# Performance work log

Measured on AMD Instinct MI355X. Metric: run time of the kernel, lower is better.

The kernel has to match this reference:

```python
import jax, jax.numpy as jnp
import numpy as np

H = 16  # num_heads
EPS = 1e-12  # F.normalize eps


def setup_inputs() -> dict:
    key = jax.random.key(0)
    ks = jax.random.split(key, 7)
    B, L, D = 2, 2048, 1024
    s = 0.02  # small init scale for numerical sanity
    return {
        "x": jax.random.normal(ks[0], (B, L, D), dtype=jnp.float32),
        "Wq": jax.random.normal(ks[1], (D, D), dtype=jnp.float32) * s,
        "Wk": jax.random.normal(ks[2], (D, D), dtype=jnp.float32) * s,
        "Wv": jax.random.normal(ks[3], (D, D), dtype=jnp.float32) * s,
        "Wo": jax.random.normal(ks[4], (D, D), dtype=jnp.float32) * s,
        "Wb": jax.random.normal(ks[5], (D, H), dtype=jnp.float32) * s,
        "bb": jnp.zeros((H,), dtype=jnp.float32),
    }


def _l2norm(t):
    # matches torch F.normalize(p=2, dim=-1): x / max(||x||, eps)
    n = jnp.sqrt(jnp.sum(t * t, axis=-1, keepdims=True))
    return t / jnp.maximum(n, EPS)


def reference(x, Wq, Wk, Wv, Wo, Wb, bb):
    B, L, Dm = x.shape
    Dh = Dm // H
    q = (x @ Wq).reshape(B, L, H, Dh)
    k = (x @ Wk).reshape(B, L, H, Dh)
    v = (x @ Wv).reshape(B, L, H, Dh)
    beta = jax.nn.sigmoid(x @ Wb + bb)  # [B, L, H]
    q = _l2norm(q)
    k = _l2norm(k)
    # out[b,l,h,e] = sum_{t<=l} beta[b,t,h] * <q[b,l,h], k[b,t,h]> * v[b,t,h,e]
    # Exact reformulation of the cumsum-of-outer-products in the source,
    # avoiding the B*L*H*Dh*Dh state blow-up.
    scores = jnp.einsum('blhd,bthd->bhlt', q, k)
    scores = scores * beta.transpose(0, 2, 1)[:, :, None, :]  # scale by beta_t
    mask = jnp.tril(jnp.ones((L, L), dtype=scores.dtype))  # causal incl. diagonal
    scores = scores * mask
    out = jnp.einsum('bhlt,bthe->blhe', scores, v).reshape(B, L, Dm)
    return out @ Wo
```

## Files before the change

kernel.cpp:

```cpp
#include <hip/hip_runtime.h>
#include <stdint.h>

#define DEV static __device__ __forceinline__

typedef __bf16 bf16x8 __attribute__((ext_vector_type(8)));
typedef unsigned short u16x8 __attribute__((ext_vector_type(8)));
typedef float f32x4 __attribute__((ext_vector_type(4)));

DEV unsigned short f2bf(float f) {
    unsigned int u = __builtin_bit_cast(unsigned int, f);
    u = (u + 0x7FFFu + ((u >> 16) & 1u)) >> 16;
    return (unsigned short)u;
}
DEV float bf2f(unsigned short h) {
    unsigned int u = ((unsigned int)h) << 16;
    return __builtin_bit_cast(float, u);
}

DEV void gload_lds16(const unsigned short* g, unsigned short* l) {
    __builtin_amdgcn_global_load_lds(
        (const __attribute__((address_space(1))) unsigned int*)g,
        (__attribute__((address_space(3))) unsigned int*)l, 16, 0, 0);
}

__global__ __launch_bounds__(256) void k_prep(
    const float* __restrict__ x, const float* __restrict__ Wq,
    const float* __restrict__ Wk, const float* __restrict__ Wv,
    const float* __restrict__ Wo, const float* __restrict__ Wb,
    const float* __restrict__ bb, unsigned short* __restrict__ xb,
    unsigned short* __restrict__ Wqkvt, unsigned short* __restrict__ Wot,
    float* __restrict__ beta) {
    __shared__ __align__(16) char smem[65536];
    int bid = blockIdx.x, tid = threadIdx.x;
    if (bid < 4096) {
        int i = bid * 256 + tid;
        float4 v = ((const float4*)x)[i];
        ushort4 o;
        o.x = f2bf(v.x); o.y = f2bf(v.y); o.z = f2bf(v.z); o.w = f2bf(v.w);
        ((ushort4*)xb)[i] = o;
    } else if (bid < 8192) {
        float (*tile)[33] = (float(*)[33])smem;
        int idx = bid - 4096;
        int z = idx >> 10, rem = idx & 1023;
        const float* W = (z == 0) ? Wq : (z == 1) ? Wk : (z == 2) ? Wv : Wo;
        int k0 = (rem & 31) * 32, n0 = (rem >> 5) * 32;
        int tx = tid & 31, ty = tid >> 5;
        #pragma unroll
        for (int r = 0; r < 32; r += 8)
            tile[ty + r][tx] = W[(size_t)(k0 + ty + r) * 1024 + n0 + tx];
        __syncthreads();
        #pragma unroll
        for (int r = 0; r < 32; r += 8) {
            float v = tile[tx][ty + r];
            int n = n0 + ty + r, k = k0 + tx;
            if (z < 3) Wqkvt[(size_t)(z * 1024 + n) * 1024 + k] = f2bf(v);
            else       Wot[(size_t)n * 1024 + k] = f2bf(v);
        }
    } else {
        float* WbT = (float*)smem;
        int bbl = bid - 8192;
        #pragma unroll
        for (int j = 0; j < 16; j++) {
            int idx4 = tid + 256 * j;
            float4 v = ((const float4*)Wb)[idx4];
            int i = idx4 >> 2;
            int h0 = (idx4 & 3) * 4;
            WbT[(h0 + 0) * 1024 + (i ^ ((h0 + 0) << 2))] = v.x;
            WbT[(h0 + 1) * 1024 + (i ^ ((h0 + 1) << 2))] = v.y;
            WbT[(h0 + 2) * 1024 + (i ^ ((h0 + 2) << 2))] = v.z;
            WbT[(h0 + 3) * 1024 + (i ^ ((h0 + 3) << 2))] = v.w;
        }
        __syncthreads();
        int w = tid >> 6, lane = tid & 63;
        #pragma unroll 1
        for (int r = 0; r < 4; r++) {
            int row = bbl * 16 + w * 4 + r;
            const float* xr = x + (size_t)row * 1024;
            float acc[16] = {};
            #pragma unroll
            for (int k = 0; k < 16; k++) {
                int i = lane + 64 * k;
                float xv = xr[i];
                #pragma unroll
                for (int h = 0; h < 16; h++)
                    acc[h] += xv * WbT[h * 1024 + (i ^ (h << 2))];
            }
            #pragma unroll
            for (int h = 0; h < 16; h++) {
                #pragma unroll
                for (int m = 32; m; m >>= 1) acc[h] += __shfl_xor(acc[h], m, 64);
            }
            if (lane == 0) {
                #pragma unroll
                for (int h = 0; h < 16; h++)
                    beta[row * 16 + h] = 1.f / (1.f + __expf(-(acc[h] + bb[h])));
            }
        }
    }
}

__global__ __launch_bounds__(256) void k_gemm_qkv(const unsigned short* __restrict__ A,
                                                  const unsigned short* __restrict__ Bt,
                                                  unsigned short* __restrict__ C) {
    __shared__ unsigned short As[128 * 32];
    __shared__ unsigned short Bs[128 * 32];
    int m0 = blockIdx.x * 128, n0 = blockIdx.y * 128;
    int tid = threadIdx.x;
    int w = tid >> 6, lane = tid & 63, g = lane >> 4, ln = lane & 15;
    int wr = w >> 1, wc = w & 1;
    f32x4 acc[4][4] = {};
    for (int k0 = 0; k0 < 1024; k0 += 32) {
        #pragma unroll
        for (int cc = 0; cc < 2; cc++) {
            int base = (w * 2 + cc) * 64;
            int chunk = base + lane;
            int row = chunk >> 2, ps = chunk & 3;
            int sl = (ps - (row >> 1)) & 3;
            gload_lds16(A + (size_t)(m0 + row) * 1024 + k0 + sl * 8, &As[base * 8]);
            gload_lds16(Bt + (size_t)(n0 + row) * 1024 + k0 + sl * 8, &Bs[base * 8]);
        }
        __syncthreads();
        bf16x8 af[4], bfr[4];
        #pragma unroll
        for (int mi = 0; mi < 4; mi++) {
            int row = wr * 64 + mi * 16 + ln;
            int ps = (g + (row >> 1)) & 3;
            af[mi] = *(const bf16x8*)(&As[row * 32 + ps * 8]);
        }
        #pragma unroll
        for (int ni = 0; ni < 4; ni++) {
            int row = wc * 64 + ni * 16 + ln;
            int ps = (g + (row >> 1)) & 3;
            bfr[ni] = *(const bf16x8*)(&Bs[row * 32 + ps * 8]);
        }
        #pragma unroll
        for (int mi = 0; mi < 4; mi++)
            #pragma unroll
            for (int ni = 0; ni < 4; ni++)
                acc[mi][ni] = __builtin_amdgcn_mfma_f32_16x16x32_bf16(
                    af[mi], bfr[ni], acc[mi][ni], 0, 0, 0);
        __syncthreads();
    }
    #pragma unroll
    for (int mi = 0; mi < 4; mi++)
        #pragma unroll
        for (int ni = 0; ni < 4; ni++)
            #pragma unroll
            for (int r = 0; r < 4; r++) {
                int row = m0 + wr * 64 + mi * 16 + g * 4 + r;
                int col = n0 + wc * 64 + ni * 16 + ln;
                C[(size_t)row * 3072 + col] = f2bf(acc[mi][ni][r]);
            }
}

__global__ __launch_bounds__(256) void k_gemm_out(const unsigned short* __restrict__ A,
                                                  const unsigned short* __restrict__ Bt,
                                                  float* __restrict__ C) {
    __shared__ unsigned short As[128 * 32];
    __shared__ unsigned short Bs[64 * 32];
    int m0 = blockIdx.x * 128, n0 = blockIdx.y * 64;
    int tid = threadIdx.x;
    int w = tid >> 6, lane = tid & 63, g = lane >> 4, ln = lane & 15;
    int wr = w >> 1, wc = w & 1;
    f32x4 acc[4][2] = {};
    for (int k0 = 0; k0 < 1024; k0 += 32) {
        #pragma unroll
        for (int i = 0; i < 3; i++) {
            int base = w * 192 + i * 64;
            int chunk = base + lane;
            if (base < 512) {
                int row = chunk >> 2, ps = chunk & 3;
                int sl = (ps - (row >> 1)) & 3;
                gload_lds16(A + (size_t)(m0 + row) * 1024 + k0 + sl * 8, &As[base * 8]);
            } else {
                int bc = chunk - 512;
                int row = bc >> 2, ps = bc & 3;
                int sl = (ps - (row >> 1)) & 3;
                gload_lds16(Bt + (size_t)(n0 + row) * 1024 + k0 + sl * 8, &Bs[(base - 512) * 8]);
            }
        }
        __syncthreads();
        bf16x8 af[4], bfr[2];
        #pragma unroll
        for (int mi = 0; mi < 4; mi++) {
            int row = wr * 64 + mi * 16 + ln;
            int ps = (g + (row >> 1)) & 3;
            af[mi] = *(const bf16x8*)(&As[row * 32 + ps * 8]);
        }
        #pragma unroll
        for (int ni = 0; ni < 2; ni++) {
            int row = wc * 32 + ni * 16 + ln;
            int ps = (g + (row >> 1)) & 3;
            bfr[ni] = *(const bf16x8*)(&Bs[row * 32 + ps * 8]);
        }
        #pragma unroll
        for (int mi = 0; mi < 4; mi++)
            #pragma unroll
            for (int ni = 0; ni < 2; ni++)
                acc[mi][ni] = __builtin_amdgcn_mfma_f32_16x16x32_bf16(
                    af[mi], bfr[ni], acc[mi][ni], 0, 0, 0);
        __syncthreads();
    }
    #pragma unroll
    for (int mi = 0; mi < 4; mi++)
        #pragma unroll
        for (int ni = 0; ni < 2; ni++)
            #pragma unroll
            for (int r = 0; r < 4; r++) {
                int row = m0 + wr * 64 + mi * 16 + g * 4 + r;
                int col = n0 + wc * 32 + ni * 16 + ln;
                C[(size_t)row * 1024 + col] = acc[mi][ni][r];
            }
}

DEV int vswz(int dh, int ks) { return (ks ^ (dh & 7) ^ ((dh >> 3) & 7)) & 7; }

__global__ __launch_bounds__(256) void k_state(const unsigned short* __restrict__ QKV,
                                               const float* __restrict__ beta,
                                               unsigned short* __restrict__ Mbuf) {
    __shared__ unsigned short Kt[64 * 64];
    __shared__ unsigned short Vt[64 * 64];
    int c = blockIdx.x, bh = blockIdx.y;
    int b = bh >> 4, h = bh & 15;
    int tid = threadIdx.x, w = tid >> 6, lane = tid & 63, g = lane >> 4, ln = lane & 15;
    int row0 = b * 2048 + c * 64;
    const unsigned short* Kg = QKV + 1024;
    const unsigned short* Vg = QKV + 2048;
    #pragma unroll
    for (int cc = 0; cc < 2; cc++) {
        int ci = tid + cc * 256;
        int r = ci >> 3, sl = ci & 7;
        uint4 kd = *(const uint4*)(Kg + (size_t)(row0 + r) * 3072 + h * 64 + sl * 8);
        uint4 vd = *(const uint4*)(Vg + (size_t)(row0 + r) * 3072 + h * 64 + sl * 8);
        union { uint4 q; unsigned short s[8]; } uk, uv;
        uk.q = kd; uv.q = vd;
        float ssk = 0.f;
        #pragma unroll
        for (int i = 0; i < 8; i++) { float v = bf2f(uk.s[i]); ssk += v * v; }
        ssk += __shfl_xor(ssk, 1, 64);
        ssk += __shfl_xor(ssk, 2, 64);
        ssk += __shfl_xor(ssk, 4, 64);
        float ksc = beta[(row0 + r) * 16 + h] / fmaxf(sqrtf(ssk), 1e-12f);
        #pragma unroll
        for (int i = 0; i < 8; i++) {
            int dh = sl * 8 + i;
            int off = dh * 64 + vswz(dh, r >> 3) * 8 + (r & 7);
            Kt[off] = f2bf(bf2f(uk.s[i]) * ksc);
            Vt[off] = uv.s[i];
        }
    }
    __syncthreads();
    f32x4 macc[4] = {};
    #pragma unroll
    for (int st = 0; st < 2; st++) {
        int c0 = st * 32 + g * 4;
        int rk = w * 16 + ln;
        uint2 klo = *(const uint2*)(&Kt[rk * 64 + vswz(rk, c0 >> 3) * 8 + (c0 & 7)]);
        uint2 khi = *(const uint2*)(&Kt[rk * 64 + vswz(rk, (c0 + 16) >> 3) * 8 + (c0 & 7)]);
        uint4 kc = make_uint4(klo.x, klo.y, khi.x, khi.y);
        bf16x8 bfrag = __builtin_bit_cast(bf16x8, kc);
        #pragma unroll
        for (int mt = 0; mt < 4; mt++) {
            int rv = mt * 16 + ln;
            uint2 lo = *(const uint2*)(&Vt[rv * 64 + vswz(rv, c0 >> 3) * 8 + (c0 & 7)]);
            uint2 hi = *(const uint2*)(&Vt[rv * 64 + vswz(rv, (c0 + 16) >> 3) * 8 + (c0 & 7)]);
            uint4 comb = make_uint4(lo.x, lo.y, hi.x, hi.y);
            bf16x8 afrag = __builtin_bit_cast(bf16x8, comb);
            macc[mt] = __builtin_amdgcn_mfma_f32_16x16x32_bf16(afrag, bfrag, macc[mt], 0, 0, 0);
        }
    }
    unsigned short* Mc = Mbuf + ((size_t)bh * 32 + c) * 4096;
    #pragma unroll
    for (int mt = 0; mt < 4; mt++)
        #pragma unroll
        for (int r = 0; r < 4; r++)
            Mc[(mt * 16 + g * 4 + r) * 64 + w * 16 + ln] = f2bf(macc[mt][r]);
}

__global__ __launch_bounds__(256) void k_prefix(unsigned short* __restrict__ Mbuf) {
    int bh = blockIdx.x >> 3, slice = blockIdx.x & 7;
    int base = slice * 512 + threadIdx.x * 2;
    unsigned short* M = Mbuf + (size_t)bh * 32 * 4096 + base;
    unsigned int v[32];
    #pragma unroll
    for (int c = 0; c < 32; c++) v[c] = *(const unsigned int*)(M + (size_t)c * 4096);
    float a0 = 0.f, a1 = 0.f;
    #pragma unroll
    for (int c = 0; c < 32; c++) {
        unsigned int pack = (unsigned int)f2bf(a0) | ((unsigned int)f2bf(a1) << 16);
        *(unsigned int*)(M + (size_t)c * 4096) = pack;
        a0 += bf2f((unsigned short)(v[c] & 0xFFFF));
        a1 += bf2f((unsigned short)(v[c] >> 16));
    }
}

__global__ __launch_bounds__(256) void k_attn2(const unsigned short* __restrict__ QKV,
                                               const unsigned short* __restrict__ Sbuf,
                                               const float* __restrict__ beta,
                                               unsigned short* __restrict__ attn) {
    __shared__ unsigned short Ks[64 * 64];
    __shared__ unsigned short Vt[64 * 64];
    __shared__ unsigned short STs[64 * 64];
    int qt = blockIdx.x, bh = blockIdx.y;
    int b = bh >> 4, h = bh & 15;
    int tid = threadIdx.x, w = tid >> 6, lane = tid & 63, g = lane >> 4, ln = lane & 15;
    int rowbase = b * 2048 + qt * 64;

    const unsigned short* Qrow = QKV + (size_t)(rowbase + w * 16 + ln) * 3072 + h * 64;
    u16x8 qu0 = *(const u16x8*)(Qrow + g * 8);
    u16x8 qu1 = *(const u16x8*)(Qrow + 32 + g * 8);
    bf16x8 qf[2];
    qf[0] = __builtin_bit_cast(bf16x8, qu0);
    qf[1] = __builtin_bit_cast(bf16x8, qu1);
    float ssq = 0.f;
    #pragma unroll
    for (int j = 0; j < 8; j++) {
        float v0 = bf2f(qu0[j]), v1 = bf2f(qu1[j]);
        ssq += v0 * v0 + v1 * v1;
    }
    ssq += __shfl_xor(ssq, 16, 64);
    ssq += __shfl_xor(ssq, 32, 64);
    float qscale = 1.f / fmaxf(sqrtf(ssq), 1e-12f);

    const unsigned short* Kg = QKV + 1024;
    const unsigned short* Vg = QKV + 2048;
    const unsigned short* Sg = Sbuf + ((size_t)bh * 32 + qt) * 4096;

    #pragma unroll
    for (int cc = 0; cc < 2; cc++) {
        int c = tid + cc * 256;
        int r = c >> 3, sl = c & 7;
        uint4 kd = *(const uint4*)(Kg + (size_t)(rowbase + r) * 3072 + h * 64 + sl * 8);
        union { uint4 q; unsigned short s[8]; } uk; uk.q = kd;
        float ssk = 0.f;
        #pragma unroll
        for (int i = 0; i < 8; i++) { float v = bf2f(uk.s[i]); ssk += v * v; }
        ssk += __shfl_xor(ssk, 1, 64);
        ssk += __shfl_xor(ssk, 2, 64);
        ssk += __shfl_xor(ssk, 4, 64);
        float ksc = beta[(rowbase + r) * 16 + h] / fmaxf(sqrtf(ssk), 1e-12f);
        #pragma unroll
        for (int i = 0; i < 8; i++) uk.s[i] = f2bf(bf2f(uk.s[i]) * ksc);
        *(uint4*)(&Ks[r * 64 + ((sl ^ (r & 7)) * 8)]) = uk.q;
        uint4 sd = *(const uint4*)(Sg + r * 64 + sl * 8);
        *(uint4*)(&STs[r * 64 + ((sl ^ (r & 7)) * 8)]) = sd;
        uint4 vd = *(const uint4*)(Vg + (size_t)(rowbase + r) * 3072 + h * 64 + sl * 8);
        union { uint4 q; unsigned short s[8]; } uv; uv.q = vd;
        #pragma unroll
        for (int i = 0; i < 8; i++) {
            int dh = sl * 8 + i;
            Vt[dh * 64 + vswz(dh, r >> 3) * 8 + (r & 7)] = uv.s[i];
        }
    }
    __syncthreads();

    f32x4 oacc[4] = {};

    #pragma unroll
    for (int st = 0; st < 2; st++)
        #pragma unroll
        for (int mt2 = 0; mt2 < 4; mt2++) {
            int r = mt2 * 16 + ln;
            int ps = (st * 4 + g) ^ (r & 7);
            bf16x8 a = *(const bf16x8*)(&STs[r * 64 + ps * 8]);
            oacc[mt2] = __builtin_amdgcn_mfma_f32_16x16x32_bf16(a, qf[st], oacc[mt2], 0, 0, 0);
        }

    f32x4 s[4] = {};
    #pragma unroll
    for (int st = 0; st < 2; st++)
        #pragma unroll
        for (int mt = 0; mt < 4; mt++) {
            int r = mt * 16 + ln;
            int ps = (st * 4 + g) ^ (r & 7);
            bf16x8 a = *(const bf16x8*)(&Ks[r * 64 + ps * 8]);
            s[mt] = __builtin_amdgcn_mfma_f32_16x16x32_bf16(a, qf[st], s[mt], 0, 0, 0);
        }
    {
        int qr = w * 16 + ln;
        #pragma unroll
        for (int mt = 0; mt < 4; mt++)
            #pragma unroll
            for (int r = 0; r < 4; r++)
                if (mt * 16 + g * 4 + r > qr) s[mt][r] = 0.f;
    }
    bf16x8 pf[2];
    #pragma unroll
    for (int st = 0; st < 2; st++) {
        u16x8 t;
        #pragma unroll
        for (int r = 0; r < 4; r++) {
            t[r]     = f2bf(s[2 * st][r]);
            t[4 + r] = f2bf(s[2 * st + 1][r]);
        }
        pf[st] = __builtin_bit_cast(bf16x8, t);
    }
    #pragma unroll
    for (int st = 0; st < 2; st++)
        #pragma unroll
        for (int mt2 = 0; mt2 < 4; mt2++) {
            int rv = mt2 * 16 + ln;
            int c0 = st * 32 + g * 4;
            uint2 lo = *(const uint2*)(&Vt[rv * 64 + vswz(rv, c0 >> 3) * 8 + (c0 & 7)]);
            uint2 hi = *(const uint2*)(&Vt[rv * 64 + vswz(rv, (c0 + 16) >> 3) * 8 + (c0 & 7)]);
            uint4 comb = make_uint4(lo.x, lo.y, hi.x, hi.y);
            bf16x8 a = __builtin_bit_cast(bf16x8, comb);
            oacc[mt2] = __builtin_amdgcn_mfma_f32_16x16x32_bf16(a, pf[st], oacc[mt2], 0, 0, 0);
        }
    __syncthreads();

    {
        int qr = w * 16 + ln;
        #pragma unroll
        for (int mt2 = 0; mt2 < 4; mt2++)
            #pragma unroll
            for (int r = 0; r < 4; r++) {
                int dh = mt2 * 16 + g * 4 + r;
                Ks[qr * 64 + (dh ^ ((qr & 7) << 3))] = f2bf(oacc[mt2][r] * qscale);
            }
    }
    __syncthreads();
    #pragma unroll
    for (int cc = 0; cc < 2; cc++) {
        int c = tid + cc * 256;
        int r = c >> 3, sl = c & 7;
        uint4 d = *(const uint4*)(&Ks[r * 64 + ((sl ^ (r & 7)) * 8)]);
        *(uint4*)(attn + (size_t)(rowbase + r) * 1024 + h * 64 + sl * 8) = d;
    }
}

extern "C" void kernel_launch(void* const* d_in, const int* in_sizes, int n_in,
                              void* d_out, int out_size, void* d_ws, size_t ws_size,
                              hipStream_t stream) {
    const float* x  = (const float*)d_in[0];
    const float* Wq = (const float*)d_in[1];
    const float* Wk = (const float*)d_in[2];
    const float* Wv = (const float*)d_in[3];
    const float* Wo = (const float*)d_in[4];
    const float* Wb = (const float*)d_in[5];
    const float* bb = (const float*)d_in[6];
    float* out = (float*)d_out;

    char* ws = (char*)d_ws;
    unsigned short* xb    = (unsigned short*)(ws);
    unsigned short* Mbuf  = (unsigned short*)(ws);
    unsigned short* Wqkvt = (unsigned short*)(ws + (8ull  << 20));
    unsigned short* Wot   = (unsigned short*)(ws + (14ull << 20));
    unsigned short* QKVb  = (unsigned short*)(ws + (16ull << 20));
    float*          beta  = (float*)         (ws + (40ull << 20));
    unsigned short* attn  = (unsigned short*)(ws + (41ull << 20));

    k_prep<<<8448, 256, 0, stream>>>(x, Wq, Wk, Wv, Wo, Wb, bb, xb, Wqkvt, Wot, beta);
    k_gemm_qkv<<<dim3(32, 24), 256, 0, stream>>>(xb, Wqkvt, QKVb);
    k_state<<<dim3(32, 32), 256, 0, stream>>>(QKVb, beta, Mbuf);
    k_prefix<<<256, 256, 0, stream>>>(Mbuf);
    k_attn2<<<dim3(32, 32), 256, 0, stream>>>(QKVb, Mbuf, beta, attn);
    k_gemm_out<<<dim3(32, 16), 256, 0, stream>>>(attn, Wot, out);
}
```

Baseline: 192.4 us.

## Split prep kernel to shrink LDS, and double GEMM K-tile to 64

Moves the beta projection out of the prep kernel into its own kernel, so the cast/transpose blocks no longer reserve 64KB of LDS and can run at higher occupancy. The beta kernel now uses one row per wave across 1024 blocks. Both GEMMs also stage 64-wide K tiles with an 8-slot swizzle, halving the barrier and loop count per K. The cost is an extra kernel launch and twice the LDS per GEMM block.

```diff
diff --git a/kernel.cpp b/kernel.cpp
--- a/kernel.cpp
+++ b/kernel.cpp
@@ -23,14 +23,12 @@
         (__attribute__((address_space(3))) unsigned int*)l, 16, 0, 0);
 }
 
-__global__ __launch_bounds__(256) void k_prep(
+__global__ __launch_bounds__(256) void k_prep0(
     const float* __restrict__ x, const float* __restrict__ Wq,
     const float* __restrict__ Wk, const float* __restrict__ Wv,
-    const float* __restrict__ Wo, const float* __restrict__ Wb,
-    const float* __restrict__ bb, unsigned short* __restrict__ xb,
-    unsigned short* __restrict__ Wqkvt, unsigned short* __restrict__ Wot,
-    float* __restrict__ beta) {
-    __shared__ __align__(16) char smem[65536];
+    const float* __restrict__ Wo, unsigned short* __restrict__ xb,
+    unsigned short* __restrict__ Wqkvt, unsigned short* __restrict__ Wot) {
+    __shared__ float tile[32][33];
     int bid = blockIdx.x, tid = threadIdx.x;
     if (bid < 4096) {
         int i = bid * 256 + tid;
@@ -38,8 +36,7 @@
         ushort4 o;
         o.x = f2bf(v.x); o.y = f2bf(v.y); o.z = f2bf(v.z); o.w = f2bf(v.w);
         ((ushort4*)xb)[i] = o;
-    } else if (bid < 8192) {
-        float (*tile)[33] = (float(*)[33])smem;
+    } else {
         int idx = bid - 4096;
         int z = idx >> 10, rem = idx & 1023;
         const float* W = (z == 0) ? Wq : (z == 1) ? Wk : (z == 2) ? Wv : Wo;
@@ -56,89 +53,94 @@
             if (z < 3) Wqkvt[(size_t)(z * 1024 + n) * 1024 + k] = f2bf(v);
             else       Wot[(size_t)n * 1024 + k] = f2bf(v);
         }
-    } else {
-        float* WbT = (float*)smem;
-        int bbl = bid - 8192;
-        #pragma unroll
-        for (int j = 0; j < 16; j++) {
-            int idx4 = tid + 256 * j;
-            float4 v = ((const float4*)Wb)[idx4];
-            int i = idx4 >> 2;
-            int h0 = (idx4 & 3) * 4;
-            WbT[(h0 + 0) * 1024 + (i ^ ((h0 + 0) << 2))] = v.x;
-            WbT[(h0 + 1) * 1024 + (i ^ ((h0 + 1) << 2))] = v.y;
-            WbT[(h0 + 2) * 1024 + (i ^ ((h0 + 2) << 2))] = v.z;
-            WbT[(h0 + 3) * 1024 + (i ^ ((h0 + 3) << 2))] = v.w;
-        }
-        __syncthreads();
-        int w = tid >> 6, lane = tid & 63;
-        #pragma unroll 1
-        for (int r = 0; r < 4; r++) {
-            int row = bbl * 16 + w * 4 + r;
-            const float* xr = x + (size_t)row * 1024;
-            float acc[16] = {};
-            #pragma unroll
-            for (int k = 0; k < 16; k++) {
-                int i = lane + 64 * k;
-                float xv = xr[i];
-                #pragma unroll
-                for (int h = 0; h < 16; h++)
-                    acc[h] += xv * WbT[h * 1024 + (i ^ (h << 2))];
-            }
-            #pragma unroll
-            for (int h = 0; h < 16; h++) {
-                #pragma unroll
-                for (int m = 32; m; m >>= 1) acc[h] += __shfl_xor(acc[h], m, 64);
-            }
-            if (lane == 0) {
-                #pragma unroll
-                for (int h = 0; h < 16; h++)
-                    beta[row * 16 + h] = 1.f / (1.f + __expf(-(acc[h] + bb[h])));
-            }
-        }
+    }
+}
+
+__global__ __launch_bounds__(256) void k_beta(const float* __restrict__ x,
+                                              const float* __restrict__ Wb,
+                                              const float* __restrict__ bb,
+                                              float* __restrict__ beta) {
+    __shared__ float WbT[16 * 1024];
+    int tid = threadIdx.x;
+    #pragma unroll
+    for (int j = 0; j < 16; j++) {
+        int idx4 = tid + 256 * j;
+        float4 v = ((const float4*)Wb)[idx4];
+        int i = idx4 >> 2;
+        int h0 = (idx4 & 3) * 4;
+        WbT[(h0 + 0) * 1024 + (i ^ ((h0 + 0) << 2))] = v.x;
+        WbT[(h0 + 1) * 1024 + (i ^ ((h0 + 1) << 2))] = v.y;
+        WbT[(h0 + 2) * 1024 + (i ^ ((h0 + 2) << 2))] = v.z;
+        WbT[(h0 + 3) * 1024 + (i ^ ((h0 + 3) << 2))] = v.w;
+    }
+    __syncthreads();
+    int w = tid >> 6, lane = tid & 63;
+    int row = blockIdx.x * 4 + w;
+    const float* xr = x + (size_t)row * 1024;
+    float acc[16] = {};
+    #pragma unroll
+    for (int k = 0; k < 16; k++) {
+        int i = lane + 64 * k;
+        float xv = xr[i];
+        #pragma unroll
+        for (int h = 0; h < 16; h++)
+            acc[h] += xv * WbT[h * 1024 + (i ^ (h << 2))];
+    }
+    #pragma unroll
+    for (int h = 0; h < 16; h++) {
+        #pragma unroll
+        for (int m = 32; m; m >>= 1) acc[h] += __shfl_xor(acc[h], m, 64);
+    }
+    if (lane == 0) {
+        #pragma unroll
+        for (int h = 0; h < 16; h++)
+            beta[row * 16 + h] = 1.f / (1.f + __expf(-(acc[h] + bb[h])));
     }
 }
 
 __global__ __launch_bounds__(256) void k_gemm_qkv(const unsigned short* __restrict__ A,
                                                   const unsigned short* __restrict__ Bt,
                                                   unsigned short* __restrict__ C) {
-    __shared__ unsigned short As[128 * 32];
-    __shared__ unsigned short Bs[128 * 32];
+    __shared__ unsigned short As[128 * 64];
+    __shared__ unsigned short Bs[128 * 64];
     int m0 = blockIdx.x * 128, n0 = blockIdx.y * 128;
     int tid = threadIdx.x;
     int w = tid >> 6, lane = tid & 63, g = lane >> 4, ln = lane & 15;
     int wr = w >> 1, wc = w & 1;
     f32x4 acc[4][4] = {};
-    for (int k0 = 0; k0 < 1024; k0 += 32) {
-        #pragma unroll
-        for (int cc = 0; cc < 2; cc++) {
-            int base = (w * 2 + cc) * 64;
+    for (int k0 = 0; k0 < 1024; k0 += 64) {
+        #pragma unroll
+        for (int cc = 0; cc < 4; cc++) {
+            int base = (w * 4 + cc) * 64;
             int chunk = base + lane;
-            int row = chunk >> 2, ps = chunk & 3;
-            int sl = (ps - (row >> 1)) & 3;
+            int row = chunk >> 3, ps = chunk & 7;
+            int sl = (ps - (row >> 1)) & 7;
             gload_lds16(A + (size_t)(m0 + row) * 1024 + k0 + sl * 8, &As[base * 8]);
             gload_lds16(Bt + (size_t)(n0 + row) * 1024 + k0 + sl * 8, &Bs[base * 8]);
         }
         __syncthreads();
-        bf16x8 af[4], bfr[4];
-        #pragma unroll
-        for (int mi = 0; mi < 4; mi++) {
-            int row = wr * 64 + mi * 16 + ln;
-            int ps = (g + (row >> 1)) & 3;
-            af[mi] = *(const bf16x8*)(&As[row * 32 + ps * 8]);
-        }
-        #pragma unroll
-        for (int ni = 0; ni < 4; ni++) {
-            int row = wc * 64 + ni * 16 + ln;
-            int ps = (g + (row >> 1)) & 3;
-            bfr[ni] = *(const bf16x8*)(&Bs[row * 32 + ps * 8]);
-        }
-        #pragma unroll
-        for (int mi = 0; mi < 4; mi++)
-            #pragma unroll
-            for (int ni = 0; ni < 4; ni++)
-                acc[mi][ni] = __builtin_amdgcn_mfma_f32_16x16x32_bf16(
-                    af[mi], bfr[ni], acc[mi][ni], 0, 0, 0);
+        #pragma unroll
+        for (int s = 0; s < 2; s++) {
+            bf16x8 af[4], bfr[4];
+            #pragma unroll
+            for (int mi = 0; mi < 4; mi++) {
+                int row = wr * 64 + mi * 16 + ln;
+                int ps = (s * 4 + g + (row >> 1)) & 7;
+                af[mi] = *(const bf16x8*)(&As[row * 64 + ps * 8]);
+            }
+            #pragma unroll
+            for (int ni = 0; ni < 4; ni++) {
+                int row = wc * 64 + ni * 16 + ln;
+                int ps = (s * 4 + g + (row >> 1)) & 7;
+                bfr[ni] = *(const bf16x8*)(&Bs[row * 64 + ps * 8]);
+            }
+            #pragma unroll
+            for (int mi = 0; mi < 4; mi++)
+                #pragma unroll
+                for (int ni = 0; ni < 4; ni++)
+                    acc[mi][ni] = __builtin_amdgcn_mfma_f32_16x16x32_bf16(
+                        af[mi], bfr[ni], acc[mi][ni], 0, 0, 0);
+        }
         __syncthreads();
     }
     #pragma unroll
@@ -156,49 +158,52 @@
 __global__ __launch_bounds__(256) void k_gemm_out(const unsigned short* __restrict__ A,
                                                   const unsigned short* __restrict__ Bt,
                                                   float* __restrict__ C) {
-    __shared__ unsigned short As[128 * 32];
-    __shared__ unsigned short Bs[64 * 32];
+    __shared__ unsigned short As[128 * 64];
+    __shared__ unsigned short Bs[64 * 64];
     int m0 = blockIdx.x * 128, n0 = blockIdx.y * 64;
     int tid = threadIdx.x;
     int w = tid >> 6, lane = tid & 63, g = lane >> 4, ln = lane & 15;
     int wr = w >> 1, wc = w & 1;
     f32x4 acc[4][2] = {};
-    for (int k0 = 0; k0 < 1024; k0 += 32) {
-        #pragma unroll
-        for (int i = 0; i < 3; i++) {
-            int base = w * 192 + i * 64;
+    for (int k0 = 0; k0 < 1024; k0 += 64) {
+        #pragma unroll
+        for (int i = 0; i < 6; i++) {
+            int base = w * 384 + i * 64;
             int chunk = base + lane;
-            if (base < 512) {
-                int row = chunk >> 2, ps = chunk & 3;
-                int sl = (ps - (row >> 1)) & 3;
+            if (base < 1024) {
+                int row = chunk >> 3, ps = chunk & 7;
+                int sl = (ps - (row >> 1)) & 7;
                 gload_lds16(A + (size_t)(m0 + row) * 1024 + k0 + sl * 8, &As[base * 8]);
             } else {
-                int bc = chunk - 512;
-                int row = bc >> 2, ps = bc & 3;
-                int sl = (ps - (row >> 1)) & 3;
-                gload_lds16(Bt + (size_t)(n0 + row) * 1024 + k0 + sl * 8, &Bs[(base - 512) * 8]);
+                int bc = chunk - 1024;
+                int row = bc >> 3, ps = bc & 7;
+                int sl = (ps - (row >> 1)) & 7;
+                gload_lds16(Bt + (size_t)(n0 + row) * 1024 + k0 + sl * 8, &Bs[(base - 1024) * 8]);
             }
         }
         __syncthreads();
-        bf16x8 af[4], bfr[2];
-        #pragma unroll
-        for (int mi = 0; mi < 4; mi++) {
-            int row = wr * 64 + mi * 16 + ln;
-            int ps = (g + (row >> 1)) & 3;
-            af[mi] = *(const bf16x8*)(&As[row * 32 + ps * 8]);
-        }
-        #pragma unroll
-        for (int ni = 0; ni < 2; ni++) {
-            int row = wc * 32 + ni * 16 + ln;
-            int ps = (g + (row >> 1)) & 3;
-            bfr[ni] = *(const bf16x8*)(&Bs[row * 32 + ps * 8]);
-        }
-        #pragma unroll
-        for (int mi = 0; mi < 4; mi++)
-            #pragma unroll
-            for (int ni = 0; ni < 2; ni++)
-                acc[mi][ni] = __builtin_amdgcn_mfma_f32_16x16x32_bf16(
-                    af[mi], bfr[ni], acc[mi][ni], 0, 0, 0);
+        #pragma unroll
+        for (int s = 0; s < 2; s++) {
+            bf16x8 af[4], bfr[2];
+            #pragma unroll
+            for (int mi = 0; mi < 4; mi++) {
+                int row = wr * 64 + mi * 16 + ln;
+                int ps = (s * 4 + g + (row >> 1)) & 7;
+                af[mi] = *(const bf16x8*)(&As[row * 64 + ps * 8]);
+            }
+            #pragma unroll
+            for (int ni = 0; ni < 2; ni++) {
+                int row = wc * 32 + ni * 16 + ln;
+                int ps = (s * 4 + g + (row >> 1)) & 7;
+                bfr[ni] = *(const bf16x8*)(&Bs[row * 64 + ps * 8]);
+            }
+            #pragma unroll
+            for (int mi = 0; mi < 4; mi++)
+                #pragma unroll
+                for (int ni = 0; ni < 2; ni++)
+                    acc[mi][ni] = __builtin_amdgcn_mfma_f32_16x16x32_bf16(
+                        af[mi], bfr[ni], acc[mi][ni], 0, 0, 0);
+        }
         __syncthreads();
     }
     #pragma unroll
@@ -450,7 +455,8 @@
     float*          beta  = (float*)         (ws + (40ull << 20));
     unsigned short* attn  = (unsigned short*)(ws + (41ull << 20));
 
-    k_prep<<<8448, 256, 0, stream>>>(x, Wq, Wk, Wv, Wo, Wb, bb, xb, Wqkvt, Wot, beta);
+    k_prep0<<<8192, 256, 0, stream>>>(x, Wq, Wk, Wv, Wo, xb, Wqkvt, Wot);
+    k_beta<<<1024, 256, 0, stream>>>(x, Wb, bb, beta);
     k_gemm_qkv<<<dim3(32, 24), 256, 0, stream>>>(xb, Wqkvt, QKVb);
     k_state<<<dim3(32, 32), 256, 0, stream>>>(QKVb, beta, Mbuf);
     k_prefix<<<256, 256, 0, stream>>>(Mbuf);
```

New measurement: 174.7 us. 9.2% less time.
